# Performance work log

Hardware: AMD Instinct MI355X
Metric: run time of the kernel (lower is better)

Reference implementation:

```python
import jax, jax.numpy as jnp
import numpy as np

# SLAYER SRM-alpha kernel: k[n] = (n/tau) * exp(1 - n/tau), k[0] = 0 (Ts = 1).
# Realized exactly as a 2-state linear recurrence instead of an explicit time conv:
#   s1[n] = r*s1[n-1] + x[n];  s2[n] = r*s2[n-1] + r*s1[n];  out[n] = (e/tau)*s2[n-1]
# which reproduces k[n] = n * r**n * e / tau for an impulse.

def _alpha_psp(x, tau):
    r = jnp.float32(np.exp(-1.0 / tau))
    coef = jnp.float32(np.e / tau)
    xT = jnp.moveaxis(x, -1, 0)  # [T,N,C,H,W]
    zeros = jnp.zeros_like(xT[0])
    def step(carry, xt):
        s1, s2 = carry
        out = coef * s2          # kernel value 0 at lag 0
        s1 = r * s1 + xt
        s2 = r * s2 + r * s1
        return (s1, s2), out
    _, out = jax.lax.scan(step, (zeros, zeros), xT)
    return jnp.moveaxis(out, 0, -1)


def _make_spike_fn(theta, tauRho, scaleRho):
    # Hard threshold forward, SLAYER exponential surrogate backward.
    @jax.custom_vjp
    def f(u):
        return (u >= theta).astype(u.dtype)
    def fwd(u):
        return f(u), u
    def bwd(u, g):
        pdf = (scaleRho / tauRho) * jnp.exp(-jnp.abs(u - theta) / (tauRho * theta))
        return (g * pdf,)
    f.defvjp(fwd, bwd)
    return f


def _spike_dynamics(u, theta, tauRef, scaleRef, tauRho, scaleRho):
    # membrane[t] = u[t] + refractory response of past spikes,
    # refKernel[n] = -scaleRef*theta * (n/tauRef) * exp(1 - n/tauRef)
    r = jnp.float32(np.exp(-1.0 / tauRef))
    coef = jnp.float32(-scaleRef * theta * np.e / tauRef)
    spike_fn = _make_spike_fn(theta, tauRho, scaleRho)
    uT = jnp.moveaxis(u, -1, 0)  # [T,N,C,H,W]
    zeros = jnp.zeros_like(uT[0])
    def step(carry, ut):
        s1, s2 = carry
        m = ut + coef * s2       # spike at t does not refract itself (kernel[0]=0)
        s = spike_fn(m)
        s1 = r * s1 + s
        s2 = r * s2 + r * s1
        return (s1, s2), s
    _, out = jax.lax.scan(step, (zeros, zeros), uT)
    return jnp.moveaxis(out, 0, -1)


def _conv2d_time(x, w, pad):
    # SLAYER conv3d with kernel (k,k,1): a 2D conv applied independently per timestep.
    N, C, H, W, T = x.shape
    xb = jnp.moveaxis(x, -1, 1).reshape(N * T, C, H, W)
    y = jax.lax.conv_general_dilated(
        xb, w, (1, 1), [(pad, pad), (pad, pad)],
        dimension_numbers=('NCHW', 'OIHW', 'NCHW'))
    return jnp.moveaxis(y.reshape(N, T, w.shape[0], H, W), 1, -1)


def setup_inputs() -> dict:
    key = jax.random.key(0)
    k1, k2, k3, k4 = jax.random.split(key, 4)
    N, C, H, W, T = 8, 4, 128, 128, 50
    spikeInput = (jax.random.uniform(k1, (N, C, H, W, T)) < 0.1).astype(jnp.float32)
    # weight scales chosen so membranes cross the per-layer thresholds (SLAYER weightScale)
    w1 = jax.random.normal(k2, (4, 4, 5, 5), jnp.float32) * 2.0
    w2 = jax.random.normal(k3, (4, 4, 3, 3), jnp.float32) * 4.0
    w3 = jax.random.normal(k4, (4, 4, 3, 3), jnp.float32) * 8.0
    return {"spikeInput": spikeInput, "w1": w1, "w2": w2, "w3": w3}


def reference(spikeInput, w1, w2, w3):
    s1 = _spike_dynamics(_conv2d_time(_alpha_psp(spikeInput, 1.0), w1, 2),
                         20.0, 1.0, 1.0, 1.0, 10.0)
    s2 = _spike_dynamics(_conv2d_time(_alpha_psp(s1, 2.0), w2, 1),
                         40.0, 2.0, 1.0, 1.0, 10.0)
    # Layer 3 is computed by the original forward but its result is NOT returned
    # (the torch code returns spikes_layer_2). XLA will DCE it.
    s3 = _spike_dynamics(_conv2d_time(_alpha_psp(s2, 4.0), w3, 1),
                         80.0, 4.0, 1.0, 10.0, 100.0)
    return s2
```

## Files before the change

### kernel.cpp

```cpp
#include <hip/hip_runtime.h>


#define TC 10

__global__ __launch_bounds__(256)
void snn_pack(const float* __restrict__ xin, uint2* __restrict__ xmg)
{
    const int i = blockIdx.x * 256 + threadIdx.x;
    const float2* p = (const float2*)(xin + (size_t)i * 50);
    unsigned m0 = 0, m1 = 0;
#pragma unroll
    for (int j = 0; j < 25; ++j) {
        float2 v = p[j];
        unsigned b0 = (v.x != 0.f) ? 1u : 0u;
        unsigned b1 = (v.y != 0.f) ? 1u : 0u;
        int k = 2 * j;
        if (k < 32) m0 |= (b0 << k) | (b1 << (k + 1));
        else        m1 |= (b0 << (k - 32)) | (b1 << (k - 31));
    }
    const int n  = i >> 16;
    const int c  = (i >> 14) & 3;
    const int yx = i & 16383;
    xmg[((size_t)((n << 14) + yx)) * 4 + c] = make_uint2(m0, m1);
}

#define HS1 20
#define HP1 21
__global__ __launch_bounds__(256)
void snn_l1(const uint2* __restrict__ xmg, const float* __restrict__ w1,
            uint2* __restrict__ s1g)
{
    __shared__ __align__(16) uint2 xs[4][HS1 * HP1];
    __shared__ __align__(16) float wL1[400];

    const int tid = threadIdx.x;
    const int n = blockIdx.z, Y0 = blockIdx.y * 16, X0 = blockIdx.x * 16;

    if (tid < 400) {
        int oc = tid & 3, r = tid >> 2;
        int ic = r / 25, r2 = r - ic * 25;
        int dy = r2 / 5, dx = r2 - dy * 5;
        wL1[tid] = w1[((oc * 4 + ic) * 5 + dy) * 5 + dx];
    }
#pragma unroll
    for (int s = 0; s < 2; ++s) {
        int hp = tid + s * 256;
        if (hp < HS1 * HS1) {
            int hy = hp / HS1, hx = hp - hy * HS1;
            int gy = Y0 + hy - 2, gx = X0 + hx - 2;
            uint4 lo = make_uint4(0, 0, 0, 0), hi = make_uint4(0, 0, 0, 0);
            if (gy >= 0 && gy < 128 && gx >= 0 && gx < 128) {
                const uint4* g = (const uint4*)
                    &xmg[((size_t)((n << 14) + gy * 128 + gx)) * 4];
                lo = g[0]; hi = g[1];
            }
            int li = hy * HP1 + hx;
            xs[0][li] = make_uint2(lo.x, lo.y);
            xs[1][li] = make_uint2(lo.z, lo.w);
            xs[2][li] = make_uint2(hi.x, hi.y);
            xs[3][li] = make_uint2(hi.z, hi.w);
        }
    }
    __syncthreads();

    const int cy = tid >> 4, cx = tid & 15;
    const int base = cy * HP1 + cx;

    float s1a[4] = {}, s2a[4] = {}, s1b[4] = {}, s2b[4] = {};
    unsigned long long om[4] = {};
    const float R1  = 0.36787944117144233f;
    const float CO1 = 2.7182818284590452f;
    const float CRF = -54.365636569180902f;

    for (int chk = 0; chk < 5; ++chk) {
        const int t0 = chk * TC;
        float a[TC][4];
#pragma unroll
        for (int u = 0; u < TC; ++u) { a[u][0]=0.f; a[u][1]=0.f; a[u][2]=0.f; a[u][3]=0.f; }
#pragma unroll 1
        for (int ic = 0; ic < 4; ++ic) {
            const uint2*  xp = &xs[ic][base];
            const float4* wp = (const float4*)&wL1[ic * 100];
#pragma unroll 1
            for (int dy = 0; dy < 5; ++dy) {
#pragma unroll
                for (int dx = 0; dx < 5; ++dx) {
                    uint2 m = xp[dx];
                    unsigned long long mm = ((unsigned long long)m.y << 32) | m.x;
                    unsigned win = (unsigned)(mm >> t0);
                    float4 w = wp[dx];
#pragma unroll
                    for (int u = 0; u < TC; ++u) {
                        float f = (float)((win >> u) & 1u);
                        a[u][0] = fmaf(f, w.x, a[u][0]);
                        a[u][1] = fmaf(f, w.y, a[u][1]);
                        a[u][2] = fmaf(f, w.z, a[u][2]);
                        a[u][3] = fmaf(f, w.w, a[u][3]);
                    }
                }
                xp += HP1; wp += 5;
            }
        }
        unsigned cm[4] = {0, 0, 0, 0};
#pragma unroll
        for (int u = 0; u < TC; ++u) {
#pragma unroll
            for (int oc = 0; oc < 4; ++oc) {
                float ao  = CO1 * s2a[oc];
                float ns1 = fmaf(R1, s1a[oc], a[u][oc]);
                s1a[oc] = ns1;
                s2a[oc] = fmaf(R1, s2a[oc], R1 * ns1);
                float mv = fmaf(CRF, s2b[oc], ao);
                unsigned b = (mv >= 20.f) ? 1u : 0u;
                float spf = (float)b;
                float nb1 = fmaf(R1, s1b[oc], spf);
                s1b[oc] = nb1;
                s2b[oc] = fmaf(R1, s2b[oc], R1 * nb1);
                cm[oc] |= b << u;
            }
        }
#pragma unroll
        for (int oc = 0; oc < 4; ++oc)
            om[oc] |= (unsigned long long)cm[oc] << t0;
    }

    uint4* g = (uint4*)&s1g[((size_t)((n << 14) + (Y0 + cy) * 128 + X0 + cx)) * 4];
    g[0] = make_uint4((unsigned)om[0], (unsigned)(om[0] >> 32),
                      (unsigned)om[1], (unsigned)(om[1] >> 32));
    g[1] = make_uint4((unsigned)om[2], (unsigned)(om[2] >> 32),
                      (unsigned)om[3], (unsigned)(om[3] >> 32));
}

#define HS2 18
#define HP2 19
__global__ __launch_bounds__(256)
void snn_l2(const uint2* __restrict__ s1g, const float* __restrict__ w2,
            float* __restrict__ out)
{
    __shared__ __align__(16) uint2 ss[4][HS2 * HP2];
    __shared__ __align__(16) float wL2[144];
    __shared__ unsigned long long oml[256 * 4];

    const int tid = threadIdx.x;
    const int n = blockIdx.z, Y0 = blockIdx.y * 16, X0 = blockIdx.x * 16;

    if (tid < 144) {
        int oc = tid & 3, r = tid >> 2;
        int ic = r / 9, r2 = r - ic * 9;
        int dy = r2 / 3, dx = r2 - dy * 3;
        wL2[tid] = w2[((oc * 4 + ic) * 3 + dy) * 3 + dx];
    }
#pragma unroll
    for (int s = 0; s < 2; ++s) {
        int hp = tid + s * 256;
        if (hp < HS2 * HS2) {
            int hy = hp / HS2, hx = hp - hy * HS2;
            int gy = Y0 + hy - 1, gx = X0 + hx - 1;
            uint4 lo = make_uint4(0, 0, 0, 0), hi = make_uint4(0, 0, 0, 0);
            if (gy >= 0 && gy < 128 && gx >= 0 && gx < 128) {
                const uint4* g = (const uint4*)
                    &s1g[((size_t)((n << 14) + gy * 128 + gx)) * 4];
                lo = g[0]; hi = g[1];
            }
            int li = hy * HP2 + hx;
            ss[0][li] = make_uint2(lo.x, lo.y);
            ss[1][li] = make_uint2(lo.z, lo.w);
            ss[2][li] = make_uint2(hi.x, hi.y);
            ss[3][li] = make_uint2(hi.z, hi.w);
        }
    }
    __syncthreads();

    const int cy = tid >> 4, cx = tid & 15;
    const int base = cy * HP2 + cx;

    float s1c[4] = {}, s2c[4] = {}, s1d[4] = {}, s2d[4] = {};
    unsigned long long om[4] = {};
    const float R2  = 0.60653065971263342f;
    const float CO2 = 1.3591409142295226f;
    const float CRF = -54.365636569180902f;

    for (int chk = 0; chk < 5; ++chk) {
        const int t0 = chk * TC;
        float a[TC][4];
#pragma unroll
        for (int u = 0; u < TC; ++u) { a[u][0]=0.f; a[u][1]=0.f; a[u][2]=0.f; a[u][3]=0.f; }
#pragma unroll 1
        for (int ic = 0; ic < 4; ++ic) {
            const uint2*  sp = &ss[ic][base];
            const float4* wp = (const float4*)&wL2[ic * 36];
#pragma unroll 1
            for (int dy = 0; dy < 3; ++dy) {
#pragma unroll
                for (int dx = 0; dx < 3; ++dx) {
                    uint2 m = sp[dx];
                    unsigned long long mm = ((unsigned long long)m.y << 32) | m.x;
                    unsigned win = (unsigned)(mm >> t0);
                    float4 w = wp[dx];
#pragma unroll
                    for (int u = 0; u < TC; ++u) {
                        float f = (float)((win >> u) & 1u);
                        a[u][0] = fmaf(f, w.x, a[u][0]);
                        a[u][1] = fmaf(f, w.y, a[u][1]);
                        a[u][2] = fmaf(f, w.z, a[u][2]);
                        a[u][3] = fmaf(f, w.w, a[u][3]);
                    }
                }
                sp += HP2; wp += 3;
            }
        }
        unsigned cm[4] = {0, 0, 0, 0};
#pragma unroll
        for (int u = 0; u < TC; ++u) {
#pragma unroll
            for (int oc = 0; oc < 4; ++oc) {
                float ao  = CO2 * s2c[oc];
                float ns1 = fmaf(R2, s1c[oc], a[u][oc]);
                s1c[oc] = ns1;
                s2c[oc] = fmaf(R2, s2c[oc], R2 * ns1);
                float mv = fmaf(CRF, s2d[oc], ao);
                unsigned b = (mv >= 40.f) ? 1u : 0u;
                float spf = (float)b;
                float nd1 = fmaf(R2, s1d[oc], spf);
                s1d[oc] = nd1;
                s2d[oc] = fmaf(R2, s2d[oc], R2 * nd1);
                cm[oc] |= b << u;
            }
        }
#pragma unroll
        for (int oc = 0; oc < 4; ++oc)
            om[oc] |= (unsigned long long)cm[oc] << t0;
    }

#pragma unroll
    for (int oc = 0; oc < 4; ++oc) oml[tid * 4 + oc] = om[oc];
    __syncthreads();

    for (int i = tid; i < 256 * 4 * 25; i += 256) {
        int pc = i / 25;
        int j  = i - pc * 25;
        int p  = pc >> 2, c = pc & 3;
        unsigned long long m = oml[p * 4 + c];
        int py = p >> 4, px = p & 15;
        int k = 2 * j;
        float2 v;
        v.x = (float)((unsigned)(m >> k) & 1u);
        v.y = (float)((unsigned)(m >> (k + 1)) & 1u);
        float* o = out + ((size_t)(((n * 4 + c) << 14) + (Y0 + py) * 128 + X0 + px)) * 50;
        *(float2*)(o + k) = v;
    }
}

#define TW   16
#define TH   8
#define R1S  (TW + 6)
#define R1R  (TH + 6)
#define R1N  (R1S * R1R)
#define R2S  (TW + 2)
#define R2R  (TH + 2)
#define R2N  (R2S * R2R)

__global__ __launch_bounds__(256)
void snn_fused_fb(const float* __restrict__ xin,
                  const float* __restrict__ w1,
                  const float* __restrict__ w2,
                  float* __restrict__ out)
{
    __shared__ __align__(16) uint2    xm[4][R1N];
    __shared__ unsigned               s1m[4][R2N];
    __shared__ __align__(16) float    wL1[400];
    __shared__ __align__(16) float    wL2[144];

    const int tid = threadIdx.x;
    const int n   = blockIdx.z;
    const int Y0  = blockIdx.y * TH;
    const int X0  = blockIdx.x * TW;

    for (int i = tid; i < 400; i += 256) {
        int oc = i & 3, r = i >> 2;
        int ic = r / 25, r2 = r - ic * 25;
        int dy = r2 / 5, dx = r2 - dy * 5;
        wL1[i] = w1[((oc * 4 + ic) * 5 + dy) * 5 + dx];
    }
    if (tid < 144) {
        int oc = tid & 3, r = tid >> 2;
        int ic = r / 9, r2 = r - ic * 9;
        int dy = r2 / 3, dx = r2 - dy * 3;
        wL2[tid] = w2[((oc * 4 + ic) * 3 + dy) * 3 + dx];
    }
#pragma unroll
    for (int s = 0; s < 2; ++s) {
        int hp = tid + s * 256;
        if (hp < R1N) {
            int hy = hp / R1S, hx = hp - hy * R1S;
            int gy = Y0 + hy - 3, gx = X0 + hx - 3;
            bool inimg = gy >= 0 && gy < 128 && gx >= 0 && gx < 128;
#pragma unroll
            for (int c = 0; c < 4; ++c) {
                unsigned m0 = 0, m1 = 0;
                if (inimg) {
                    const float2* p = (const float2*)
                        (xin + ((size_t)(((n * 4 + c) * 128 + gy) * 128 + gx)) * 50);
#pragma unroll
                    for (int j = 0; j < 25; ++j) {
                        float2 v = p[j];
                        unsigned b0 = (v.x != 0.f) ? 1u : 0u;
                        unsigned b1 = (v.y != 0.f) ? 1u : 0u;
                        int k = 2 * j;
                        if (k < 32) m0 |= (b0 << k) | (b1 << (k + 1));
                        else        m1 |= (b0 << (k - 32)) | (b1 << (k - 31));
                    }
                }
                xm[c][hp] = make_uint2(m0, m1);
            }
        }
    }
    const bool cw = (tid < R2N);
    const int cy = tid / R2S;
    const int cx = tid - cy * R2S;
    const bool cin = cw && (Y0 + cy - 1) >= 0 && (Y0 + cy - 1) < 128
                        && (X0 + cx - 1) >= 0 && (X0 + cx - 1) < 128;
    const int xbase = cy * R1S + cx;
    const bool iw = (tid < TW * TH);
    const int iy = tid >> 4, ix = tid & 15;
    const int ibase = iy * R2S + ix;

    float s1a[4] = {}, s2a[4] = {}, s1b[4] = {}, s2b[4] = {};
    float s1c[4] = {}, s2c[4] = {}, s1d[4] = {}, s2d[4] = {};
    unsigned long long om[4] = {};

    const float R1  = 0.36787944117144233f;
    const float CO1 = 2.7182818284590452f;
    const float R2  = 0.60653065971263342f;
    const float CO2 = 1.3591409142295226f;
    const float CRF = -54.365636569180902f;

    __syncthreads();

    for (int chk = 0; chk < 5; ++chk) {
        const int t0 = chk * TC;
        if (cw) {
            float a[TC][4];
#pragma unroll
            for (int u = 0; u < TC; ++u) { a[u][0]=0.f; a[u][1]=0.f; a[u][2]=0.f; a[u][3]=0.f; }
            if (cin) {
#pragma unroll 1
                for (int ic = 0; ic < 4; ++ic) {
                    const uint2*  xp = &xm[ic][xbase];
                    const float4* wp = (const float4*)&wL1[ic * 100];
#pragma unroll 1
                    for (int dy = 0; dy < 5; ++dy) {
#pragma unroll
                        for (int dx = 0; dx < 5; ++dx) {
                            uint2 m = xp[dx];
                            unsigned long long mm =
                                ((unsigned long long)m.y << 32) | m.x;
                            unsigned win = (unsigned)(mm >> t0);
                            float4 w = wp[dx];
#pragma unroll
                            for (int u = 0; u < TC; ++u) {
                                float f = (float)((win >> u) & 1u);
                                a[u][0] = fmaf(f, w.x, a[u][0]);
                                a[u][1] = fmaf(f, w.y, a[u][1]);
                                a[u][2] = fmaf(f, w.z, a[u][2]);
                                a[u][3] = fmaf(f, w.w, a[u][3]);
                            }
                        }
                        xp += R1S; wp += 5;
                    }
                }
            }
            unsigned cm[4] = {0, 0, 0, 0};
#pragma unroll
            for (int u = 0; u < TC; ++u) {
#pragma unroll
                for (int oc = 0; oc < 4; ++oc) {
                    float ao  = CO1 * s2a[oc];
                    float ns1 = fmaf(R1, s1a[oc], a[u][oc]);
                    s1a[oc] = ns1;
                    s2a[oc] = fmaf(R1, s2a[oc], R1 * ns1);
                    float mv = fmaf(CRF, s2b[oc], ao);
                    unsigned b = (mv >= 20.f) ? 1u : 0u;
                    float spf = (float)b;
                    float nb1 = fmaf(R1, s1b[oc], spf);
                    s1b[oc] = nb1;
                    s2b[oc] = fmaf(R1, s2b[oc], R1 * nb1);
                    cm[oc] |= b << u;
                }
            }
            s1m[0][tid] = cm[0];
            s1m[1][tid] = cm[1];
            s1m[2][tid] = cm[2];
            s1m[3][tid] = cm[3];
        }
        __syncthreads();
        if (iw) {
            float a[TC][4];
#pragma unroll
            for (int u = 0; u < TC; ++u) { a[u][0]=0.f; a[u][1]=0.f; a[u][2]=0.f; a[u][3]=0.f; }
#pragma unroll 1
            for (int ic = 0; ic < 4; ++ic) {
                const unsigned* sp = &s1m[ic][ibase];
                const float4*   wp = (const float4*)&wL2[ic * 36];
#pragma unroll 1
                for (int dy = 0; dy < 3; ++dy) {
#pragma unroll
                    for (int dx = 0; dx < 3; ++dx) {
                        unsigned win = sp[dx];
                        float4 w = wp[dx];
#pragma unroll
                        for (int u = 0; u < TC; ++u) {
                            float f = (float)((win >> u) & 1u);
                            a[u][0] = fmaf(f, w.x, a[u][0]);
                            a[u][1] = fmaf(f, w.y, a[u][1]);
                            a[u][2] = fmaf(f, w.z, a[u][2]);
                            a[u][3] = fmaf(f, w.w, a[u][3]);
                        }
                    }
                    sp += R2S; wp += 3;
                }
            }
            unsigned cm[4] = {0, 0, 0, 0};
#pragma unroll
            for (int u = 0; u < TC; ++u) {
#pragma unroll
                for (int oc = 0; oc < 4; ++oc) {
                    float ao  = CO2 * s2c[oc];
                    float ns1 = fmaf(R2, s1c[oc], a[u][oc]);
                    s1c[oc] = ns1;
                    s2c[oc] = fmaf(R2, s2c[oc], R2 * ns1);
                    float mv = fmaf(CRF, s2d[oc], ao);
                    unsigned b = (mv >= 40.f) ? 1u : 0u;
                    float spf = (float)b;
                    float nd1 = fmaf(R2, s1d[oc], spf);
                    s1d[oc] = nd1;
                    s2d[oc] = fmaf(R2, s2d[oc], R2 * nd1);
                    cm[oc] |= b << u;
                }
            }
#pragma unroll
            for (int oc = 0; oc < 4; ++oc)
                om[oc] |= (unsigned long long)cm[oc] << t0;
        }
        __syncthreads();
    }
    if (iw) {
#pragma unroll
        for (int c = 0; c < 4; ++c) {
            float* p = out + ((size_t)(((n * 4 + c) * 128 + (Y0 + iy)) * 128 + (X0 + ix))) * 50;
            unsigned long long m = om[c];
#pragma unroll
            for (int j = 0; j < 25; ++j) {
                int k = 2 * j;
                float2 v;
                v.x = (float)((unsigned)(m >> k) & 1u);
                v.y = (float)((unsigned)(m >> (k + 1)) & 1u);
                *(float2*)(p + k) = v;
            }
        }
    }
}

extern "C" void kernel_launch(void* const* d_in, const int* in_sizes, int n_in,
                              void* d_out, int out_size, void* d_ws, size_t ws_size,
                              hipStream_t stream) {
    (void)in_sizes; (void)n_in; (void)out_size;
    const float* x  = (const float*)d_in[0];
    const float* w1 = (const float*)d_in[1];
    const float* w2 = (const float*)d_in[2];
    float* o = (float*)d_out;

    if (ws_size >= 2u * 4194304u) {
        uint2* xmg = (uint2*)d_ws;
        uint2* s1g = xmg + 524288;
        hipLaunchKernelGGL(snn_pack, dim3(2048), dim3(256), 0, stream, x, xmg);
        hipLaunchKernelGGL(snn_l1, dim3(8, 8, 8), dim3(256), 0, stream, xmg, w1, s1g);
        hipLaunchKernelGGL(snn_l2, dim3(8, 8, 8), dim3(256), 0, stream, s1g, w2, o);
    } else {
        dim3 grid(128 / TW, 128 / TH, 8);
        hipLaunchKernelGGL(snn_fused_fb, grid, dim3(256), 0, stream, x, w1, w2, o);
    }
}
```

Baseline: 312.0 us.

## Pack spike bits with wave ballots and store bitmasks channel-planar

The pack kernel now has each wave read its 64x50 block of floats with contiguous lane accesses and build bit masks through __ballot, instead of each thread reading its own 50-float strided row. The bits are staged in shared memory and then rearranged into per-pixel 50-bit masks. The packed layouts for input and layer-1 spikes change from pixel-interleaved channels to channel-planar NCHW, and the l1/l2 halo loads and the l1 store are updated to match. The goal is coalesced reads of the large float input, at the cost of four separate 8-byte loads per halo pixel in place of two 16-byte loads.

After: 326.3 us. +4.6%, slower.

```diff
diff --git a/kernel.cpp b/kernel.cpp
--- a/kernel.cpp
+++ b/kernel.cpp
@@ -6,22 +6,25 @@
 __global__ __launch_bounds__(256)
 void snn_pack(const float* __restrict__ xin, uint2* __restrict__ xmg)
 {
-    const int i = blockIdx.x * 256 + threadIdx.x;
-    const float2* p = (const float2*)(xin + (size_t)i * 50);
-    unsigned m0 = 0, m1 = 0;
-#pragma unroll
-    for (int j = 0; j < 25; ++j) {
-        float2 v = p[j];
-        unsigned b0 = (v.x != 0.f) ? 1u : 0u;
-        unsigned b1 = (v.y != 0.f) ? 1u : 0u;
-        int k = 2 * j;
-        if (k < 32) m0 |= (b0 << k) | (b1 << (k + 1));
-        else        m1 |= (b0 << (k - 32)) | (b1 << (k - 31));
-    }
-    const int n  = i >> 16;
-    const int c  = (i >> 14) & 3;
-    const int yx = i & 16383;
-    xmg[((size_t)((n << 14) + yx)) * 4 + c] = make_uint2(m0, m1);
+    __shared__ unsigned long long bal[4][50];
+    const int tid  = threadIdx.x;
+    const int lane = tid & 63;
+    const int ws   = tid >> 6;
+    const size_t wpx = ((size_t)blockIdx.x * 4 + ws) * 64;
+    const float* src = xin + wpx * 50;
+#pragma unroll 1
+    for (int j = 0; j < 50; ++j) {
+        float v = src[j * 64 + lane];
+        unsigned long long b = __ballot(v != 0.f);
+        if (lane == 0) bal[ws][j] = b;
+    }
+    __syncthreads();
+    const int bitpos = lane * 50;
+    const int w = bitpos >> 6, s = bitpos & 63;
+    unsigned long long m = bal[ws][w] >> s;
+    if (s > 14) m |= bal[ws][w + 1] << (64 - s);
+    m &= (1ull << 50) - 1;
+    xmg[wpx + lane] = make_uint2((unsigned)m, (unsigned)(m >> 32));
 }
 
 #define HS1 20
@@ -36,11 +39,11 @@
     const int tid = threadIdx.x;
     const int n = blockIdx.z, Y0 = blockIdx.y * 16, X0 = blockIdx.x * 16;
 
-    if (tid < 400) {
-        int oc = tid & 3, r = tid >> 2;
+    for (int i = tid; i < 400; i += 256) {
+        int oc = i & 3, r = i >> 2;
         int ic = r / 25, r2 = r - ic * 25;
         int dy = r2 / 5, dx = r2 - dy * 5;
-        wL1[tid] = w1[((oc * 4 + ic) * 5 + dy) * 5 + dx];
+        wL1[i] = w1[((oc * 4 + ic) * 5 + dy) * 5 + dx];
     }
 #pragma unroll
     for (int s = 0; s < 2; ++s) {
@@ -48,17 +51,15 @@
         if (hp < HS1 * HS1) {
             int hy = hp / HS1, hx = hp - hy * HS1;
             int gy = Y0 + hy - 2, gx = X0 + hx - 2;
-            uint4 lo = make_uint4(0, 0, 0, 0), hi = make_uint4(0, 0, 0, 0);
-            if (gy >= 0 && gy < 128 && gx >= 0 && gx < 128) {
-                const uint4* g = (const uint4*)
-                    &xmg[((size_t)((n << 14) + gy * 128 + gx)) * 4];
-                lo = g[0]; hi = g[1];
-            }
+            bool ok = gy >= 0 && gy < 128 && gx >= 0 && gx < 128;
+            int gi = (gy << 7) + gx;
             int li = hy * HP1 + hx;
-            xs[0][li] = make_uint2(lo.x, lo.y);
-            xs[1][li] = make_uint2(lo.z, lo.w);
-            xs[2][li] = make_uint2(hi.x, hi.y);
-            xs[3][li] = make_uint2(hi.z, hi.w);
+#pragma unroll
+            for (int c = 0; c < 4; ++c) {
+                uint2 v = make_uint2(0u, 0u);
+                if (ok) v = xmg[(((size_t)(n * 4 + c)) << 14) + gi];
+                xs[c][li] = v;
+            }
         }
     }
     __syncthreads();
@@ -85,8 +86,8 @@
             for (int dy = 0; dy < 5; ++dy) {
 #pragma unroll
                 for (int dx = 0; dx < 5; ++dx) {
-                    uint2 m = xp[dx];
-                    unsigned long long mm = ((unsigned long long)m.y << 32) | m.x;
+                    uint2 mv = xp[dx];
+                    unsigned long long mm = ((unsigned long long)mv.y << 32) | mv.x;
                     unsigned win = (unsigned)(mm >> t0);
                     float4 w = wp[dx];
 #pragma unroll
@@ -124,11 +125,11 @@
             om[oc] |= (unsigned long long)cm[oc] << t0;
     }
 
-    uint4* g = (uint4*)&s1g[((size_t)((n << 14) + (Y0 + cy) * 128 + X0 + cx)) * 4];
-    g[0] = make_uint4((unsigned)om[0], (unsigned)(om[0] >> 32),
-                      (unsigned)om[1], (unsigned)(om[1] >> 32));
-    g[1] = make_uint4((unsigned)om[2], (unsigned)(om[2] >> 32),
-                      (unsigned)om[3], (unsigned)(om[3] >> 32));
+    const int yx = (Y0 + cy) * 128 + X0 + cx;
+#pragma unroll
+    for (int oc = 0; oc < 4; ++oc)
+        s1g[(((size_t)(n * 4 + oc)) << 14) + yx] =
+            make_uint2((unsigned)om[oc], (unsigned)(om[oc] >> 32));
 }
 
 #define HS2 18
@@ -156,17 +157,15 @@
         if (hp < HS2 * HS2) {
             int hy = hp / HS2, hx = hp - hy * HS2;
             int gy = Y0 + hy - 1, gx = X0 + hx - 1;
-            uint4 lo = make_uint4(0, 0, 0, 0), hi = make_uint4(0, 0, 0, 0);
-            if (gy >= 0 && gy < 128 && gx >= 0 && gx < 128) {
-                const uint4* g = (const uint4*)
-                    &s1g[((size_t)((n << 14) + gy * 128 + gx)) * 4];
-                lo = g[0]; hi = g[1];
-            }
+            bool ok = gy >= 0 && gy < 128 && gx >= 0 && gx < 128;
+            int gi = (gy << 7) + gx;
             int li = hy * HP2 + hx;
-            ss[0][li] = make_uint2(lo.x, lo.y);
-            ss[1][li] = make_uint2(lo.z, lo.w);
-            ss[2][li] = make_uint2(hi.x, hi.y);
-            ss[3][li] = make_uint2(hi.z, hi.w);
+#pragma unroll
+            for (int c = 0; c < 4; ++c) {
+                uint2 v = make_uint2(0u, 0u);
+                if (ok) v = s1g[(((size_t)(n * 4 + c)) << 14) + gi];
+                ss[c][li] = v;
+            }
         }
     }
     __syncthreads();
@@ -193,8 +192,8 @@
             for (int dy = 0; dy < 3; ++dy) {
 #pragma unroll
                 for (int dx = 0; dx < 3; ++dx) {
-                    uint2 m = sp[dx];
-                    unsigned long long mm = ((unsigned long long)m.y << 32) | m.x;
+                    uint2 mv = sp[dx];
+                    unsigned long long mm = ((unsigned long long)mv.y << 32) | mv.x;
                     unsigned win = (unsigned)(mm >> t0);
                     float4 w = wp[dx];
 #pragma unroll
```
